# Kernel tuning notes

Measured on AMD Instinct MI355X. Metric: run time of the kernel, lower is better.

Reference implementation:

```python
import jax, jax.numpy as jnp
import numpy as np

N_QUBITS = 4
N_LAYERS = 3
LETTERS = "ijkl"  # one axis label per qubit; batch axis is 'b'
CNOT = np.array([[1, 0, 0, 0], [0, 1, 0, 0], [0, 0, 0, 1], [0, 0, 1, 0]], dtype=np.complex64).reshape(2, 2, 2, 2)


def _apply_1q(state, U, w, batched):
    # state: [B,2,2,2,2]; U: [2,2] (shared) or [B,2,2] (per-sample)
    s = "b" + LETTERS
    t = LETTERS[w]
    u = ("b" if batched else "") + "z" + t
    return jnp.einsum(f"{u},{s}->{s.replace(t, 'z')}", U, state)


def _apply_cnot(state, c, t):
    s = "b" + LETTERS
    a, b = LETTERS[c], LETTERS[t]
    out = s.replace(a, "x").replace(b, "y")
    return jnp.einsum(f"xy{a}{b},{s}->{out}", jnp.asarray(CNOT), state)


def _rx(theta):
    # theta: [B] -> batched RX gates [B,2,2]
    c = jnp.cos(theta / 2).astype(jnp.complex64)
    s = (-1j * jnp.sin(theta / 2)).astype(jnp.complex64)
    return jnp.stack([jnp.stack([c, s], -1), jnp.stack([s, c], -1)], -2)


def _rz(a):
    e = jnp.exp(-1j * a.astype(jnp.complex64) / 2)
    zero = jnp.zeros((), jnp.complex64)
    return jnp.array([[e, zero], [zero, jnp.conj(e)]])


def _ry(a):
    c = jnp.cos(a / 2).astype(jnp.complex64)
    s = jnp.sin(a / 2).astype(jnp.complex64)
    return jnp.array([[c, -s], [s, c]])


def _rot(phi, theta, omega):
    # PennyLane Rot = RZ(omega) @ RY(theta) @ RZ(phi)
    return _rz(omega) @ _ry(theta) @ _rz(phi)


def _circuit(qparams, z):
    # qparams: [n_layers, n_qubits, 3] float32; z: [B, n_qubits] float32
    B = z.shape[0]
    state = jnp.zeros((B,) + (2,) * N_QUBITS, jnp.complex64)
    state = state.at[:, 0, 0, 0, 0].set(1.0 + 0.0j)
    # data-encoding RX layer (per-sample angles -> batched gates)
    for w in range(N_QUBITS):
        state = _apply_1q(state, _rx(z[:, w]), w, batched=True)
    # variational layers: Rot on every wire then CNOT ladder
    for layer in range(N_LAYERS):
        for w in range(N_QUBITS):
            U = _rot(qparams[layer, w, 0], qparams[layer, w, 1], qparams[layer, w, 2])
            state = _apply_1q(state, U, w, batched=False)
        for w in range(N_QUBITS - 1):
            state = _apply_cnot(state, w, w + 1)
    probs = jnp.abs(state) ** 2  # [B,2,2,2,2] float32
    zsign = jnp.array([1.0, -1.0], jnp.float32)
    s = "b" + LETTERS
    evs = [jnp.einsum(f"{s},{LETTERS[w]}->b", probs, zsign) for w in range(N_QUBITS)]
    return jnp.stack(evs, axis=-1)  # [B, n_qubits]


def reference(x, enc_w, enc_b, qparams, cls_w, cls_b, bn_gamma, bn_beta):
    B = x.shape[0]
    # avg_pool2d(kernel_size=6) on 28x28 -> 4x4 (floor division drops last 4 rows/cols)
    pooled = x[:, :, :24, :24].reshape(B, 1, 4, 6, 4, 6).mean(axis=(3, 5)).reshape(B, 16)
    z = pooled @ enc_w.T + enc_b  # [B, n_qubits]
    evs = _circuit(qparams, z)    # [B, n_qubits]
    out = evs @ cls_w.T + cls_b   # [B, output_dim]
    # BatchNorm1d in training mode: biased batch statistics, eps=1e-5
    mu = out.mean(axis=0)
    var = ((out - mu) ** 2).mean(axis=0)
    out = (out - mu) / jnp.sqrt(var + 1e-5) * bn_gamma + bn_beta
    return out


def setup_inputs() -> dict:
    key = jax.random.key(0)
    ks = jax.random.split(key, 6)
    B = 32768
    return {
        "x": jax.random.normal(ks[0], (B, 1, 28, 28), jnp.float32),
        "enc_w": jax.random.normal(ks[1], (N_QUBITS, 16), jnp.float32) * 0.25,
        "enc_b": jnp.zeros((N_QUBITS,), jnp.float32),
        "qparams": jax.random.normal(ks[2], (N_LAYERS, N_QUBITS, 3), jnp.float32),
        "cls_w": jax.random.normal(ks[3], (4, N_QUBITS), jnp.float32) * 0.5,
        "cls_b": jnp.zeros((4,), jnp.float32),
        "bn_gamma": jnp.ones((4,), jnp.float32),
        "bn_beta": jnp.zeros((4,), jnp.float32),
    }
```

## Files before the change

### kernel.cpp

```cpp
#include <hip/hip_runtime.h>
#include <math.h>


#define BTOT 32768
#define SPB  16
#define NBLK (BTOT / SPB)
#define SSTR 576

__device__ float g_partials[NBLK * 8];

__global__ __launch_bounds__(256) void fused_kernel(
    const float* __restrict__ x,
    const float* __restrict__ enc_w, const float* __restrict__ enc_b,
    const float* __restrict__ qparams, const float* __restrict__ cls_w,
    const float* __restrict__ cls_b,
    float* __restrict__ preBN)
{
    __shared__ float sx[SPB * SSTR];
    __shared__ float sVr[16 * 17];
    __shared__ float sVi[16 * 17];
    __shared__ float sW2[4 * 17];
    __shared__ float red[4][8];

    const int tid = threadIdx.x;
    const int s0  = blockIdx.x * SPB;
    const float4* xb = (const float4*)x;

    {
        const int waveBase = tid & ~63;
        #pragma unroll
        for (int it = 0; it < 9; ++it) {
            const int gid  = it * 256 + tid;
            const int c    = gid / 144;
            const int o    = gid - c * 144;
            const int row  = o / 6;
            const int col4 = o - row * 6;
            const float4* gsrc = xb + (size_t)(s0 + c) * 196 + row * 7 + col4;
            float* lbase = &sx[(it * 256 + waveBase) * 4];
            __builtin_amdgcn_global_load_lds(
                (const __attribute__((address_space(1))) void*)gsrc,
                (__attribute__((address_space(3))) void*)lbase,
                16, 0, 0);
        }
    }

    if (tid < 64) {
        {
            int j = tid >> 4, i = tid & 15;
            float acc = 0.f;
            #pragma unroll
            for (int w = 0; w < 4; ++w)
                acc += cls_w[j * 4 + w] * ((i & (8 >> w)) ? -1.f : 1.f);
            sW2[j * 17 + i] = acc;
        }
        if (tid < 16) {
            const int t = tid;
            float pr[16], pi[16];
            #pragma unroll
            for (int i = 0; i < 16; ++i) { pr[i] = (i == t) ? 1.f : 0.f; pi[i] = 0.f; }
            #pragma unroll
            for (int layer = 0; layer < 3; ++layer) {
                #pragma unroll
                for (int w = 0; w < 4; ++w) {
                    const float* qp = qparams + (layer * 4 + w) * 3;
                    float phi = qp[0], th = qp[1], om = qp[2];
                    float c, s, ca, sa, cd, sd;
                    __sincosf(0.5f * th, &s, &c);
                    __sincosf(0.5f * (phi + om), &sa, &ca);
                    __sincosf(0.5f * (phi - om), &sd, &cd);
                    float u00r =  c * ca, u00i = -c * sa;
                    float u01r = -s * cd, u01i = -s * sd;
                    float u10r =  s * cd, u10i = -s * sd;
                    float u11r =  c * ca, u11i =  c * sa;
                    const int m = 8 >> w;
                    #pragma unroll
                    for (int idx = 0; idx < 16; ++idx) {
                        if (idx & m) continue;
                        const int i1 = idx | m;
                        float ar = pr[idx], ai = pi[idx], br = pr[i1], bi = pi[i1];
                        pr[idx] = u00r*ar - u00i*ai + u01r*br - u01i*bi;
                        pi[idx] = u00r*ai + u00i*ar + u01r*bi + u01i*br;
                        pr[i1]  = u10r*ar - u10i*ai + u11r*br - u11i*bi;
                        pi[i1]  = u10r*ai + u10i*ar + u11r*bi + u11i*br;
                    }
                }
                #pragma unroll
                for (int w = 0; w < 3; ++w) {
                    const int mc = 8 >> w, mt = 8 >> (w + 1);
                    #pragma unroll
                    for (int idx = 0; idx < 16; ++idx) {
                        if ((idx & mc) && !(idx & mt)) {
                            const int i1 = idx | mt;
                            float tr = pr[idx], ti = pi[idx];
                            pr[idx] = pr[i1]; pi[idx] = pi[i1];
                            pr[i1] = tr;      pi[i1] = ti;
                        }
                    }
                }
            }
            const int p = __popc(t) & 3;
            #pragma unroll
            for (int i = 0; i < 16; ++i) {
                float re = pr[i], im = pi[i], vr, vi;
                if (p == 0)      { vr = re;  vi = im;  }
                else if (p == 1) { vr = im;  vi = -re; }
                else if (p == 2) { vr = -re; vi = -im; }
                else             { vr = -im; vi = re;  }
                sVr[i * 17 + t] = vr;
                sVi[i * 17 + t] = vi;
            }
        }
    }
    __syncthreads();

    const int s = tid >> 4, cell = tid & 15;
    const int cr = cell >> 2, cc = cell & 3;
    int srot = s;
    srot -= (srot >= 12) ? 12 : ((srot >= 6) ? 6 : 0);
    const float* sb = &sx[s * SSTR + cr * 6 * 24 + cc * 6];
    float sum = 0.f;
    #pragma unroll
    for (int rr = 0; rr < 6; ++rr) {
        int r = rr + srot; r -= (r >= 6) ? 6 : 0;
        const float2* rp = (const float2*)(sb + r * 24);
        float2 a = rp[0], b = rp[1], c2 = rp[2];
        sum += (a.x + a.y) + (b.x + b.y) + (c2.x + c2.y);
    }
    const float pv = sum * (1.f / 36.f);

    float z[4];
    #pragma unroll
    for (int j = 0; j < 4; ++j) z[j] = enc_w[j * 16 + cell] * pv;
    #pragma unroll
    for (int m = 1; m <= 8; m <<= 1) {
        #pragma unroll
        for (int j = 0; j < 4; ++j) z[j] += __shfl_xor(z[j], m, 64);
    }
    #pragma unroll
    for (int j = 0; j < 4; ++j) z[j] += enc_b[j];

    float cz[4], sz[4];
    #pragma unroll
    for (int j = 0; j < 4; ++j) __sincosf(0.5f * z[j], &sz[j], &cz[j]);
    float a01[4] = {cz[0]*cz[1], cz[0]*sz[1], sz[0]*cz[1], sz[0]*sz[1]};
    float a23[4] = {cz[2]*cz[3], cz[2]*sz[3], sz[2]*cz[3], sz[2]*sz[3]};
    float rv[16];
    #pragma unroll
    for (int k = 0; k < 16; ++k) rv[k] = a01[k >> 2] * a23[k & 3];

    float ar = 0.f, ai = 0.f;
    #pragma unroll
    for (int k = 0; k < 16; ++k) {
        ar += sVr[cell * 17 + k] * rv[k];
        ai += sVi[cell * 17 + k] * rv[k];
    }
    const float prob = ar * ar + ai * ai;
    float out[4];
    #pragma unroll
    for (int j = 0; j < 4; ++j) out[j] = sW2[j * 17 + cell] * prob;
    #pragma unroll
    for (int m = 1; m <= 8; m <<= 1) {
        #pragma unroll
        for (int j = 0; j < 4; ++j) out[j] += __shfl_xor(out[j], m, 64);
    }
    #pragma unroll
    for (int j = 0; j < 4; ++j) out[j] += cls_b[j];

    if (cell == 0)
        ((float4*)preBN)[s0 + s] = make_float4(out[0], out[1], out[2], out[3]);

    const float w = (cell == 0) ? 1.f : 0.f;
    float v8[8] = {out[0]*w, out[1]*w, out[2]*w, out[3]*w,
                   out[0]*out[0]*w, out[1]*out[1]*w, out[2]*out[2]*w, out[3]*out[3]*w};
    #pragma unroll
    for (int m = 0; m < 8; ++m) {
        v8[m] += __shfl_down(v8[m], 32, 64);
        v8[m] += __shfl_down(v8[m], 16, 64);
    }
    const int wave = tid >> 6, lane = tid & 63;
    if (lane == 0) {
        #pragma unroll
        for (int m = 0; m < 8; ++m) red[wave][m] = v8[m];
    }
    __syncthreads();
    if (tid < 8)
        g_partials[blockIdx.x * 8 + tid] =
            red[0][tid] + red[1][tid] + red[2][tid] + red[3][tid];
}

__global__ __launch_bounds__(256) void bn_kernel(
    const float* __restrict__ gamma, const float* __restrict__ beta,
    float* __restrict__ out)
{
    const int tid = threadIdx.x;
    float acc[8] = {0, 0, 0, 0, 0, 0, 0, 0};
    const float4* p4 = (const float4*)g_partials;
    #pragma unroll
    for (int it = 0; it < NBLK / 256; ++it) {
        int b = it * 256 + tid;
        float4 a = p4[b * 2], c = p4[b * 2 + 1];
        acc[0] += a.x; acc[1] += a.y; acc[2] += a.z; acc[3] += a.w;
        acc[4] += c.x; acc[5] += c.y; acc[6] += c.z; acc[7] += c.w;
    }
    #pragma unroll
    for (int off = 32; off >= 1; off >>= 1) {
        #pragma unroll
        for (int m = 0; m < 8; ++m) acc[m] += __shfl_xor(acc[m], off, 64);
    }
    __shared__ float red[4][8];
    const int wave = tid >> 6, lane = tid & 63;
    if (lane == 0) {
        #pragma unroll
        for (int m = 0; m < 8; ++m) red[wave][m] = acc[m];
    }
    __syncthreads();
    float sums[8];
    #pragma unroll
    for (int m = 0; m < 8; ++m)
        sums[m] = red[0][m] + red[1][m] + red[2][m] + red[3][m];

    const int s = blockIdx.x * 256 + tid;
    const float invB = 1.f / (float)BTOT;
    float4 v = ((const float4*)out)[s];
    float o[4] = {v.x, v.y, v.z, v.w};
    #pragma unroll
    for (int j = 0; j < 4; ++j) {
        float mu   = sums[j] * invB;
        float var  = sums[4 + j] * invB - mu * mu;
        float rstd = rsqrtf(var + 1e-5f);
        o[j] = (o[j] - mu) * rstd * gamma[j] + beta[j];
    }
    ((float4*)out)[s] = make_float4(o[0], o[1], o[2], o[3]);
}

extern "C" void kernel_launch(void* const* d_in, const int* in_sizes, int n_in,
                              void* d_out, int out_size, void* d_ws, size_t ws_size,
                              hipStream_t stream)
{
    const float* x        = (const float*)d_in[0];
    const float* enc_w    = (const float*)d_in[1];
    const float* enc_b    = (const float*)d_in[2];
    const float* qparams  = (const float*)d_in[3];
    const float* cls_w    = (const float*)d_in[4];
    const float* cls_b    = (const float*)d_in[5];
    const float* bn_gamma = (const float*)d_in[6];
    const float* bn_beta  = (const float*)d_in[7];

    float* outp = (float*)d_out;
    (void)d_ws; (void)ws_size;

    fused_kernel<<<NBLK, 256, 0, stream>>>(x, enc_w, enc_b, qparams, cls_w,
                                           cls_b, outp);
    bn_kernel<<<128, 256, 0, stream>>>(bn_gamma, bn_beta, outp);
}
```

Before: 179.8 us.

## Process four sample chunks per block with double-buffered async LDS staging

Each block now handles four chunks of 16 samples instead of one, so the grid shrinks by a factor of four. The input tile for the next chunk is loaded into a second LDS buffer while the current chunk is computed, using explicit vmcnt waits and barriers. This amortizes the per-block circuit matrix setup and overlaps global loads with compute. In exchange it doubles the LDS footprint, which can lower occupancy, and adds manual waitcnt sequencing that must match the issued load count.

Measured after the change: 173.7 us. -3.4%, faster.

```diff
diff --git a/kernel.cpp b/kernel.cpp
--- a/kernel.cpp
+++ b/kernel.cpp
@@ -4,10 +4,11 @@
 
 #define BTOT 32768
 #define SPB  16
-#define NBLK (BTOT / SPB)
+#define NC   4
+#define FB   (BTOT / (SPB * NC))
 #define SSTR 576
 
-__device__ float g_partials[NBLK * 8];
+__device__ float g_partials[FB * 8];
 
 __global__ __launch_bounds__(256) void fused_kernel(
     const float* __restrict__ x,
@@ -16,18 +17,18 @@
     const float* __restrict__ cls_b,
     float* __restrict__ preBN)
 {
-    __shared__ float sx[SPB * SSTR];
+    __shared__ __align__(16) float sx[2][SPB * SSTR];
     __shared__ float sVr[16 * 17];
     __shared__ float sVi[16 * 17];
     __shared__ float sW2[4 * 17];
     __shared__ float red[4][8];
 
-    const int tid = threadIdx.x;
-    const int s0  = blockIdx.x * SPB;
+    const int tid   = threadIdx.x;
+    const int sBase = blockIdx.x * (SPB * NC);
     const float4* xb = (const float4*)x;
-
-    {
-        const int waveBase = tid & ~63;
+    const int waveBase = tid & ~63;
+
+    auto STAGE = [&](int buf, int smp0) {
         #pragma unroll
         for (int it = 0; it < 9; ++it) {
             const int gid  = it * 256 + tid;
@@ -35,14 +36,16 @@
             const int o    = gid - c * 144;
             const int row  = o / 6;
             const int col4 = o - row * 6;
-            const float4* gsrc = xb + (size_t)(s0 + c) * 196 + row * 7 + col4;
-            float* lbase = &sx[(it * 256 + waveBase) * 4];
+            const float4* gsrc = xb + (size_t)(smp0 + c) * 196 + row * 7 + col4;
+            float* lbase = &sx[buf][(it * 256 + waveBase) * 4];
             __builtin_amdgcn_global_load_lds(
                 (const __attribute__((address_space(1))) void*)gsrc,
                 (__attribute__((address_space(3))) void*)lbase,
                 16, 0, 0);
         }
-    }
+    };
+
+    STAGE(0, sBase);
 
     if (tid < 64) {
         {
@@ -111,76 +114,104 @@
             }
         }
     }
-    __syncthreads();
 
     const int s = tid >> 4, cell = tid & 15;
     const int cr = cell >> 2, cc = cell & 3;
     int srot = s;
     srot -= (srot >= 12) ? 12 : ((srot >= 6) ? 6 : 0);
-    const float* sb = &sx[s * SSTR + cr * 6 * 24 + cc * 6];
-    float sum = 0.f;
-    #pragma unroll
-    for (int rr = 0; rr < 6; ++rr) {
-        int r = rr + srot; r -= (r >= 6) ? 6 : 0;
-        const float2* rp = (const float2*)(sb + r * 24);
-        float2 a = rp[0], b = rp[1], c2 = rp[2];
-        sum += (a.x + a.y) + (b.x + b.y) + (c2.x + c2.y);
-    }
-    const float pv = sum * (1.f / 36.f);
-
-    float z[4];
-    #pragma unroll
-    for (int j = 0; j < 4; ++j) z[j] = enc_w[j * 16 + cell] * pv;
-    #pragma unroll
-    for (int m = 1; m <= 8; m <<= 1) {
-        #pragma unroll
-        for (int j = 0; j < 4; ++j) z[j] += __shfl_xor(z[j], m, 64);
-    }
-    #pragma unroll
-    for (int j = 0; j < 4; ++j) z[j] += enc_b[j];
-
-    float cz[4], sz[4];
-    #pragma unroll
-    for (int j = 0; j < 4; ++j) __sincosf(0.5f * z[j], &sz[j], &cz[j]);
-    float a01[4] = {cz[0]*cz[1], cz[0]*sz[1], sz[0]*cz[1], sz[0]*sz[1]};
-    float a23[4] = {cz[2]*cz[3], cz[2]*sz[3], sz[2]*cz[3], sz[2]*sz[3]};
-    float rv[16];
-    #pragma unroll
-    for (int k = 0; k < 16; ++k) rv[k] = a01[k >> 2] * a23[k & 3];
-
-    float ar = 0.f, ai = 0.f;
-    #pragma unroll
-    for (int k = 0; k < 16; ++k) {
-        ar += sVr[cell * 17 + k] * rv[k];
-        ai += sVi[cell * 17 + k] * rv[k];
-    }
-    const float prob = ar * ar + ai * ai;
-    float out[4];
-    #pragma unroll
-    for (int j = 0; j < 4; ++j) out[j] = sW2[j * 17 + cell] * prob;
-    #pragma unroll
-    for (int m = 1; m <= 8; m <<= 1) {
-        #pragma unroll
-        for (int j = 0; j < 4; ++j) out[j] += __shfl_xor(out[j], m, 64);
-    }
-    #pragma unroll
-    for (int j = 0; j < 4; ++j) out[j] += cls_b[j];
-
-    if (cell == 0)
-        ((float4*)preBN)[s0 + s] = make_float4(out[0], out[1], out[2], out[3]);
-
-    const float w = (cell == 0) ? 1.f : 0.f;
-    float v8[8] = {out[0]*w, out[1]*w, out[2]*w, out[3]*w,
-                   out[0]*out[0]*w, out[1]*out[1]*w, out[2]*out[2]*w, out[3]*out[3]*w};
+    float ew[4], eb[4], cb[4];
+    #pragma unroll
+    for (int j = 0; j < 4; ++j) {
+        ew[j] = enc_w[j * 16 + cell];
+        eb[j] = enc_b[j];
+        cb[j] = cls_b[j];
+    }
+    float acc8[8] = {0, 0, 0, 0, 0, 0, 0, 0};
+
+    #pragma unroll
+    for (int t = 0; t < NC; ++t) {
+        if (t < NC - 1) STAGE((t + 1) & 1, sBase + (t + 1) * SPB);
+        if (t < NC - 1) asm volatile("s_waitcnt vmcnt(9) lgkmcnt(0)" ::: "memory");
+        else            asm volatile("s_waitcnt vmcnt(0) lgkmcnt(0)" ::: "memory");
+        __builtin_amdgcn_s_barrier();
+        __builtin_amdgcn_sched_barrier(0);
+
+        const float* sb = &sx[t & 1][s * SSTR + cr * 6 * 24 + cc * 6];
+        float sum = 0.f;
+        #pragma unroll
+        for (int rr = 0; rr < 6; ++rr) {
+            int r = rr + srot; r -= (r >= 6) ? 6 : 0;
+            const float2* rp = (const float2*)(sb + r * 24);
+            float2 a = rp[0], b = rp[1], c2 = rp[2];
+            sum += (a.x + a.y) + (b.x + b.y) + (c2.x + c2.y);
+        }
+        const float pv = sum * (1.f / 36.f);
+
+        float z[4];
+        #pragma unroll
+        for (int j = 0; j < 4; ++j) z[j] = ew[j] * pv;
+        #pragma unroll
+        for (int m = 1; m <= 8; m <<= 1) {
+            #pragma unroll
+            for (int j = 0; j < 4; ++j) z[j] += __shfl_xor(z[j], m, 64);
+        }
+        #pragma unroll
+        for (int j = 0; j < 4; ++j) z[j] += eb[j];
+
+        float cz[4], sz[4];
+        #pragma unroll
+        for (int j = 0; j < 4; ++j) __sincosf(0.5f * z[j], &sz[j], &cz[j]);
+        float a01[4] = {cz[0]*cz[1], cz[0]*sz[1], sz[0]*cz[1], sz[0]*sz[1]};
+        float a23[4] = {cz[2]*cz[3], cz[2]*sz[3], sz[2]*cz[3], sz[2]*sz[3]};
+        float rv[16];
+        #pragma unroll
+        for (int k = 0; k < 16; ++k) rv[k] = a01[k >> 2] * a23[k & 3];
+
+        float ar = 0.f, ai = 0.f;
+        #pragma unroll
+        for (int k = 0; k < 16; ++k) {
+            ar += sVr[cell * 17 + k] * rv[k];
+            ai += sVi[cell * 17 + k] * rv[k];
+        }
+        const float prob = ar * ar + ai * ai;
+        float out[4];
+        #pragma unroll
+        for (int j = 0; j < 4; ++j) out[j] = sW2[j * 17 + cell] * prob;
+        #pragma unroll
+        for (int m = 1; m <= 8; m <<= 1) {
+            #pragma unroll
+            for (int j = 0; j < 4; ++j) out[j] += __shfl_xor(out[j], m, 64);
+        }
+        #pragma unroll
+        for (int j = 0; j < 4; ++j) out[j] += cb[j];
+
+        if (cell == 0)
+            ((float4*)preBN)[sBase + t * SPB + s] =
+                make_float4(out[0], out[1], out[2], out[3]);
+
+        const float w = (cell == 0) ? 1.f : 0.f;
+        #pragma unroll
+        for (int j = 0; j < 4; ++j) {
+            acc8[j]     += out[j] * w;
+            acc8[4 + j] += out[j] * out[j] * w;
+        }
+
+        if (t < NC - 1) {
+            __builtin_amdgcn_sched_barrier(0);
+            __builtin_amdgcn_s_barrier();
+            __builtin_amdgcn_sched_barrier(0);
+        }
+    }
+
     #pragma unroll
     for (int m = 0; m < 8; ++m) {
-        v8[m] += __shfl_down(v8[m], 32, 64);
-        v8[m] += __shfl_down(v8[m], 16, 64);
+        acc8[m] += __shfl_down(acc8[m], 32, 64);
+        acc8[m] += __shfl_down(acc8[m], 16, 64);
     }
     const int wave = tid >> 6, lane = tid & 63;
     if (lane == 0) {
         #pragma unroll
-        for (int m = 0; m < 8; ++m) red[wave][m] = v8[m];
+        for (int m = 0; m < 8; ++m) red[wave][m] = acc8[m];
     }
     __syncthreads();
     if (tid < 8)
@@ -196,7 +227,7 @@
     float acc[8] = {0, 0, 0, 0, 0, 0, 0, 0};
     const float4* p4 = (const float4*)g_partials;
     #pragma unroll
-    for (int it = 0; it < NBLK / 256; ++it) {
+    for (int it = 0; it < FB / 256; ++it) {
         int b = it * 256 + tid;
         float4 a = p4[b * 2], c = p4[b * 2 + 1];
         acc[0] += a.x; acc[1] += a.y; acc[2] += a.z; acc[3] += a.w;
@@ -249,7 +280,7 @@
     float* outp = (float*)d_out;
     (void)d_ws; (void)ws_size;
 
-    fused_kernel<<<NBLK, 256, 0, stream>>>(x, enc_w, enc_b, qparams, cls_w,
-                                           cls_b, outp);
+    fused_kernel<<<FB, 256, 0, stream>>>(x, enc_w, enc_b, qparams, cls_w,
+                                         cls_b, outp);
     bn_kernel<<<128, 256, 0, stream>>>(bn_gamma, bn_beta, outp);
 }
```
